# Performance work log

Hardware: AMD Instinct MI355X
Metric: run time of the kernel (lower is better)

## Reference

```python
import jax, jax.numpy as jnp
import numpy as np
from itertools import combinations

SEQ_LEN = 8
FEAT = 2048
SET_SIZE = 2
DOUT = 1152
WAY = 5
SHOT = 5
NQ = 500
MAX_LEN = int(SEQ_LEN * 1.5)
LN_EPS = 1e-5

TUPLES = np.array(list(combinations(range(SEQ_LEN), SET_SIZE)), dtype=np.int32)  # [T, SET_SIZE]
T_LEN = TUPLES.shape[0]  # C(8,2) = 28

def _positional_encoding(d_model, max_len):
    pos = np.arange(max_len, dtype=np.float32)[:, None]
    div = np.exp(np.arange(0, d_model, 2, dtype=np.float32) * (-np.log(10000.0) / d_model))
    pe = np.zeros((max_len, d_model), dtype=np.float32)
    pe[:, 0::2] = np.sin(pos * div)
    pe[:, 1::2] = np.cos(pos * div)
    return jnp.asarray(pe)

PE = _positional_encoding(FEAT, MAX_LEN)  # dropout is identity in eval mode

def _layernorm(x, gamma, beta):
    mu = jnp.mean(x, axis=-1, keepdims=True)
    var = jnp.var(x, axis=-1, keepdims=True)
    return (x - mu) * jax.lax.rsqrt(var + LN_EPS) * gamma + beta

def setup_inputs() -> dict:
    key = jax.random.key(0)
    ks = jax.random.split(key, 8)
    din = FEAT * SET_SIZE
    sc = 1.0 / np.sqrt(din)
    return {
        "support_set": jax.random.normal(ks[0], (WAY * SHOT, SEQ_LEN, FEAT), jnp.float32),
        "support_labels": jnp.repeat(jnp.arange(WAY, dtype=jnp.int32), SHOT),  # sorted, balanced episode
        "queries": jax.random.normal(ks[1], (NQ, SEQ_LEN, FEAT), jnp.float32),
        "k_w": jax.random.normal(ks[2], (din, DOUT), jnp.float32) * sc,
        "k_b": jnp.zeros((DOUT,), jnp.float32),
        "v_w": jax.random.normal(ks[3], (din, DOUT), jnp.float32) * sc,
        "v_b": jnp.zeros((DOUT,), jnp.float32),
        "ln_k_gamma": jnp.ones((DOUT,), jnp.float32),
        "ln_k_beta": jnp.zeros((DOUT,), jnp.float32),
        "global_temperature": jnp.asarray(1.0, jnp.float32),
        "temperature_weight": jnp.ones((1,), jnp.float32),
    }

def reference(support_set, support_labels, queries, k_w, k_b, v_w, v_b,
              ln_k_gamma, ln_k_beta, global_temperature, temperature_weight):
    n_q = queries.shape[0]
    # positional encoding (dropout is eval-mode identity)
    s = support_set + PE[:SEQ_LEN]
    q = queries + PE[:SEQ_LEN]
    # gather frame tuples: [n, T, SET_SIZE, FEAT] -> [n, T, SET_SIZE*FEAT]
    s_t = s[:, TUPLES, :].reshape(WAY * SHOT, T_LEN, SET_SIZE * FEAT)
    q_t = q[:, TUPLES, :].reshape(n_q, T_LEN, SET_SIZE * FEAT)
    # K / V projections; LayerNorm only on K (as in the module)
    s_ks = _layernorm(s_t @ k_w + k_b, ln_k_gamma, ln_k_beta)
    q_ks = _layernorm(q_t @ k_w + k_b, ln_k_gamma, ln_k_beta)
    s_vs = s_t @ v_w + v_b
    q_vs = q_t @ v_w + v_b
    # labels are sorted & balanced -> per-class slices are a reshape
    class_k = s_ks.reshape(WAY, SHOT, T_LEN, DOUT)
    class_v = s_vs.reshape(WAY, SHOT, T_LEN, DOUT)
    # scores[c,q,t,k,u] = <q_ks[q,t], class_k[c,k,u]> / sqrt(DOUT)
    scores = jnp.einsum('qtd,ckud->cqtku', q_ks, class_k) / np.sqrt(DOUT)
    # softmax jointly over (support-clip k, support-tuple u) per query tuple t
    attn = jax.nn.softmax(scores.reshape(WAY, n_q, T_LEN, SHOT * T_LEN), axis=-1)
    attn = attn.reshape(WAY, n_q, T_LEN, SHOT, T_LEN)
    # prototype = sum over support clips of attn @ class_v
    proto = jnp.einsum('cqtku,ckud->cqtd', attn, class_v)  # [WAY, NQ, T, DOUT]
    diff = q_vs[None] - proto
    dist = jnp.sum(diff * diff, axis=(-2, -1)) / T_LEN  # [WAY, NQ]
    logits = (-dist * global_temperature * temperature_weight[0]).T  # [NQ, WAY]
    return logits
```

## Files before the change

kernel.cpp:

```cpp
#include <hip/hip_runtime.h>

typedef __bf16 bf16;
typedef __attribute__((ext_vector_type(8))) __bf16 bf16x8;
typedef __attribute__((ext_vector_type(4))) float f32x4;

#define AS1 __attribute__((address_space(1)))
#define AS3 __attribute__((address_space(3)))

__device__ __constant__ int c_T0[28] = {0,0,0,0,0,0,0,1,1,1,1,1,1,2,2,2,2,2,3,3,3,3,4,4,4,5,5,6};
__device__ __constant__ int c_T1[28] = {1,2,3,4,5,6,7,2,3,4,5,6,7,3,4,5,6,7,4,5,6,7,5,6,7,6,7,7};

__global__ __launch_bounds__(256) void fill_pack(
    const float* __restrict__ queries, const float* __restrict__ support,
    const float* __restrict__ kw, const float* __restrict__ vw,
    bf16* __restrict__ X, bf16* __restrict__ Wp)
{
    __shared__ float t[32][33];
    const int tid = threadIdx.x;
    if (blockIdx.x < 4224) {
        const int f = blockIdx.x;
        bf16* row = X + (long)f * 2048;
        const int d0 = tid << 3;
        if (f >= 4200) {
            bf16x8 z;
            #pragma unroll
            for (int i = 0; i < 8; ++i) z[i] = (bf16)0.f;
            *(bf16x8*)(row + d0) = z;
            return;
        }
        const float* src = (f < 4000) ? (queries + (long)f * 2048)
                                      : (support + (long)(f - 4000) * 2048);
        const int s = f & 7;
        bf16x8 o;
        #pragma unroll
        for (int i = 0; i < 8; ++i) {
            int d = d0 + i;
            float dv = __expf((float)(d >> 1) * -0.008994473019508f);
            float ang = (float)s * dv;
            float pe = (d & 1) ? __cosf(ang) : __sinf(ang);
            o[i] = (bf16)(src[d] + pe);
        }
        *(bf16x8*)(row + d0) = o;
    } else {
        const int b = blockIdx.x - 4224;
        const int k0 = (b & 63) << 5, n0g = (b >> 6) << 5;
        const int tx = tid & 31, ty = tid >> 5;
        const int j = n0g / 1152, nc = n0g % 1152;
        const float* src = ((j < 2) ? kw : vw) + (long)(((j & 1) << 11) + k0) * 1152 + nc;
        #pragma unroll
        for (int i = 0; i < 4; ++i)
            t[ty + (i << 3)][tx] = src[(long)(ty + (i << 3)) * 1152 + tx];
        __syncthreads();
        #pragma unroll
        for (int i = 0; i < 4; ++i)
            Wp[(long)(n0g + ty + (i << 3)) * 2048 + k0 + tx] = (bf16)t[tx][ty + (i << 3)];
    }
}

template <typename OutT>
__global__ __launch_bounds__(256) void gemm_bt(
    const bf16* __restrict__ A, const bf16* __restrict__ A2,
    const bf16* __restrict__ A3, int split1, int split2,
    long lda, long lda3, const bf16* __restrict__ B, long ldb,
    OutT* __restrict__ C, int N, int K, float scale, int tiles_n)
{
    __shared__ __align__(16) bf16 lA[128 * 32];
    __shared__ __align__(16) bf16 lB[128 * 32];
    const int tid = threadIdx.x;
    const int wid = tid >> 6, lane = tid & 63;
    const int wm = (wid >> 1) << 6, wn = (wid & 1) << 6;
    const int quad = lane >> 4, l16 = lane & 15;
    const int nbm = gridDim.x / tiles_n;
    const int grp = 8 * tiles_n;
    const int gid = blockIdx.x / grp;
    const int first = gid << 3;
    const int gsz = min(8, nbm - first);
    const int pig = blockIdx.x % grp;
    const int tm = first + (pig % gsz);
    const int tn = pig / gsz;
    const int m0 = tm << 7, n0 = tn << 7;
    long la = lda;
    const bf16* Abase;
    if (tm < split1)       Abase = A  + (long)m0 * lda;
    else if (tm < split2)  Abase = A2 + (long)(m0 - (split1 << 7)) * lda;
    else                 { Abase = A3 + (long)(m0 - (split2 << 7)) * lda3; la = lda3; }

    f32x4 acc[4][4];
    #pragma unroll
    for (int i = 0; i < 4; ++i)
        #pragma unroll
        for (int j = 0; j < 4; ++j)
            #pragma unroll
            for (int r = 0; r < 4; ++r) acc[i][j][r] = 0.f;

    const int srow = lane >> 2, scol = (lane & 3) << 3;
    for (int kk = 0; kk < K; kk += 32) {
        __syncthreads();
        #pragma unroll
        for (int p = 0; p < 2; ++p) {
            const int rbase = (wid << 5) + (p << 4);
            const bf16* ga = Abase + (long)(rbase + srow) * la + kk + scol;
            const bf16* gb = B + (long)(n0 + rbase + srow) * ldb + kk + scol;
            __builtin_amdgcn_global_load_lds((const AS1 unsigned int*)ga,
                                             (AS3 unsigned int*)(lA + rbase * 32), 16, 0, 0);
            __builtin_amdgcn_global_load_lds((const AS1 unsigned int*)gb,
                                             (AS3 unsigned int*)(lB + rbase * 32), 16, 0, 0);
        }
        __builtin_amdgcn_s_waitcnt(0);
        __syncthreads();
        bf16x8 af[4], bfr[4];
        #pragma unroll
        for (int i = 0; i < 4; ++i)
            af[i] = *(const bf16x8*)(lA + (wm + (i << 4) + l16) * 32 + (quad << 3));
        #pragma unroll
        for (int j = 0; j < 4; ++j)
            bfr[j] = *(const bf16x8*)(lB + (wn + (j << 4) + l16) * 32 + (quad << 3));
        #pragma unroll
        for (int i = 0; i < 4; ++i)
            #pragma unroll
            for (int j = 0; j < 4; ++j)
                acc[i][j] = __builtin_amdgcn_mfma_f32_16x16x32_bf16(af[i], bfr[j], acc[i][j], 0, 0, 0);
    }
    #pragma unroll
    for (int i = 0; i < 4; ++i) {
        const int row = m0 + wm + (i << 4) + (quad << 2);
        #pragma unroll
        for (int j = 0; j < 4; ++j) {
            const int col = n0 + wn + (j << 4) + l16;
            OutT* cp = C + (long)row * N + col;
            #pragma unroll
            for (int r = 0; r < 4; ++r) cp[(long)r * N] = (OutT)(acc[i][j][r] * scale);
        }
    }
}

__global__ __launch_bounds__(256) void proj_rows(
    const bf16* __restrict__ H, const float* __restrict__ kb,
    const float* __restrict__ vb, const float* __restrict__ gamma,
    const float* __restrict__ beta,
    bf16* __restrict__ qks, bf16* __restrict__ sks, bf16* __restrict__ svs)
{
    const int bid = blockIdx.x, tid = threadIdx.x;
    bf16 *outK, *outV = nullptr;
    int fi = 0, fj = 0;
    bool valid;
    if (bid < 14080) {
        outK = qks + (long)bid * 1152;
        valid = (bid < 14000);
        if (valid) {
            int q = bid / 28, t = bid - q * 28;
            fi = (q << 3) + c_T0[t];
            fj = (q << 3) + c_T1[t];
        }
    } else {
        int m2 = bid - 14080;
        outK = sks + (long)m2 * 1152;
        outV = svs + (long)m2 * 1152;
        valid = (m2 < 700);
        if (valid) {
            int n = m2 / 28, t = m2 - n * 28;
            fi = 4000 + (n << 3) + c_T0[t];
            fj = 4000 + (n << 3) + c_T1[t];
        }
    }
    if (!valid) {
        for (int d = tid; d < 1152; d += 256) {
            outK[d] = (bf16)0.f;
            if (outV) outV[d] = (bf16)0.f;
        }
        return;
    }
    const bf16* Hi = H + (long)fi * 4608;
    const bf16* Hj = H + (long)fj * 4608;
    float xv[5];
    float sum = 0.f, sumsq = 0.f;
    #pragma unroll
    for (int it = 0; it < 5; ++it) {
        int d = tid + (it << 8);
        float x = 0.f;
        if (d < 1152) {
            x = (float)Hi[d] + (float)Hj[1152 + d] + kb[d];
            sum += x; sumsq += x * x;
        }
        xv[it] = x;
    }
    #pragma unroll
    for (int off = 32; off > 0; off >>= 1) {
        sum += __shfl_xor(sum, off, 64);
        sumsq += __shfl_xor(sumsq, off, 64);
    }
    __shared__ float s1[4], s2[4];
    const int wid = tid >> 6;
    if ((tid & 63) == 0) { s1[wid] = sum; s2[wid] = sumsq; }
    __syncthreads();
    sum = s1[0] + s1[1] + s1[2] + s1[3];
    sumsq = s2[0] + s2[1] + s2[2] + s2[3];
    const float mu = sum * (1.f / 1152.f);
    const float var = sumsq * (1.f / 1152.f) - mu * mu;
    const float rs = rsqrtf(var + 1e-5f);
    #pragma unroll
    for (int it = 0; it < 5; ++it) {
        int d = tid + (it << 8);
        if (d < 1152) outK[d] = (bf16)((xv[it] - mu) * rs * gamma[d] + beta[d]);
    }
    if (outV) {
        #pragma unroll
        for (int it = 0; it < 5; ++it) {
            int d = tid + (it << 8);
            if (d < 1152) outV[d] = (bf16)((float)Hi[2304 + d] + (float)Hj[3456 + d] + vb[d]);
        }
    }
}

__global__ __launch_bounds__(256) void qs_pair(
    const bf16* __restrict__ H, const float* __restrict__ vb, float* __restrict__ QS)
{
    const int q = blockIdx.x, tid = threadIdx.x;
    __shared__ __align__(16) bf16 Vt[8 * 1152];
    __shared__ __align__(16) bf16 Vb[8 * 1152];
    __shared__ float dots[64];
    for (int idx = tid; idx < 1152; idx += 256) {
        int row = idx / 144, col = (idx - row * 144) << 3;
        const bf16* src = H + (long)((q << 3) + row) * 4608;
        *(bf16x8*)(Vt + row * 1152 + col) = *(const bf16x8*)(src + 2304 + col);
        *(bf16x8*)(Vb + row * 1152 + col) = *(const bf16x8*)(src + 3456 + col);
    }
    __syncthreads();
    const int wid = tid >> 6, lane = tid & 63;
    for (int task = wid; task <= 60; task += 4) {
        float s = 0.f;
        if (task == 60) {
            for (int c = lane << 3; c < 1152; c += 512) {
                #pragma unroll
                for (int k = 0; k < 8; ++k) { float v = vb[c + k]; s += v * v; }
            }
        } else if (task < 16) {
            const bf16* p = (task < 8) ? (Vt + task * 1152) : (Vb + (task - 8) * 1152);
            for (int c = lane << 3; c < 1152; c += 512) {
                bf16x8 v = *(const bf16x8*)(p + c);
                #pragma unroll
                for (int k = 0; k < 8; ++k) { float f = (float)v[k]; s += f * f; }
            }
        } else if (task < 32) {
            const bf16* p = (task < 24) ? (Vt + (task - 16) * 1152) : (Vb + (task - 24) * 1152);
            for (int c = lane << 3; c < 1152; c += 512) {
                bf16x8 v = *(const bf16x8*)(p + c);
                #pragma unroll
                for (int k = 0; k < 8; ++k) s += (float)v[k] * vb[c + k];
            }
        } else {
            int t = task - 32;
            const bf16* pa = Vt + c_T0[t] * 1152;
            const bf16* pb = Vb + c_T1[t] * 1152;
            for (int c = lane << 3; c < 1152; c += 512) {
                bf16x8 a = *(const bf16x8*)(pa + c);
                bf16x8 b = *(const bf16x8*)(pb + c);
                #pragma unroll
                for (int k = 0; k < 8; ++k) s += (float)a[k] * (float)b[k];
            }
        }
        #pragma unroll
        for (int off = 32; off > 0; off >>= 1) s += __shfl_xor(s, off, 64);
        if (lane == 0) dots[task] = s;
    }
    __syncthreads();
    if (tid < 64) {
        float term = 0.f;
        if (lane < 28) {
            int i = c_T0[lane], j = c_T1[lane];
            term = dots[i] + dots[8 + j] + dots[60]
                 + 2.f * (dots[32 + lane] + dots[16 + i] + dots[24 + j]);
        }
        #pragma unroll
        for (int off = 32; off > 0; off >>= 1) term += __shfl_xor(term, off, 64);
        if (lane == 0) QS[q] = term;
    }
}

__global__ __launch_bounds__(256) void small_ops(
    const float* __restrict__ Gf, bf16* __restrict__ Gb,
    const float* __restrict__ vb, const bf16* __restrict__ svs,
    float* __restrict__ bdot)
{
    if (blockIdx.x < 2304) {
        int i = blockIdx.x * 256 + threadIdx.x;
        int r = i / 768, col = i - r * 768;
        bool keep = (r < 700) && (col < 700) && (r / 140 == col / 140);
        Gb[i] = keep ? (bf16)Gf[i] : (bf16)0.f;
    } else {
        const int u = ((blockIdx.x - 2304) << 2) + (threadIdx.x >> 6);
        const int lane = threadIdx.x & 63;
        const bf16* p = svs + (long)u * 1152;
        float s = 0.f;
        for (int d = lane; d < 1152; d += 64) s += vb[d] * (float)p[d];
        #pragma unroll
        for (int off = 32; off > 0; off >>= 1) s += __shfl_xor(s, off, 64);
        if (lane == 0) bdot[u] = s;
    }
}

__global__ __launch_bounds__(320) void softmax_attn(
    const float* __restrict__ scores, bf16* __restrict__ attn)
{
    const int m = blockIdx.x, tid = threadIdx.x;
    bf16* arow = attn + (long)m * 768;
    if (m >= 14000) {
        for (int d = tid; d < 768; d += 320) arow[d] = (bf16)0.f;
        return;
    }
    if (tid < 68) arow[700 + tid] = (bf16)0.f;
    const int w = tid >> 6, lane = tid & 63;
    const float* srow = scores + (long)m * 768 + w * 140;
    float v0 = srow[lane];
    float v1 = srow[64 + lane];
    float v2 = (lane < 12) ? srow[128 + lane] : -1e30f;
    float mx = fmaxf(fmaxf(v0, v1), v2);
    #pragma unroll
    for (int off = 32; off > 0; off >>= 1) mx = fmaxf(mx, __shfl_xor(mx, off, 64));
    float e0 = __expf(v0 - mx), e1 = __expf(v1 - mx);
    float e2 = (lane < 12) ? __expf(v2 - mx) : 0.f;
    float s = e0 + e1 + e2;
    #pragma unroll
    for (int off = 32; off > 0; off >>= 1) s += __shfl_xor(s, off, 64);
    const float inv = 1.f / s;
    bf16* aw = arow + w * 140;
    aw[lane] = (bf16)(e0 * inv);
    aw[64 + lane] = (bf16)(e1 * inv);
    if (lane < 12) aw[128 + lane] = (bf16)(e2 * inv);
}

__global__ __launch_bounds__(256) void final_dist(
    const bf16* __restrict__ attn, const bf16* __restrict__ attnG,
    const float* __restrict__ Fv, const float* __restrict__ bdot,
    float* __restrict__ dist)
{
    const int w = threadIdx.x >> 6, lane = threadIdx.x & 63;
    const int m = blockIdx.x * 4 + w;
    const int q = m / 28, t = m - q * 28;
    const int fi = (q << 3) + c_T0[t], fj = (q << 3) + c_T1[t];
    const bf16* ar = attn + (long)m * 768;
    const bf16* gr = attnG + (long)m * 768;
    const float* ft = Fv + (long)fi * 768;
    const float* fb = Fv + (long)(4224 + fj) * 768;
    #pragma unroll
    for (int c = 0; c < 5; ++c) {
        const int base = c * 140;
        float s = 0.f;
        {
            int u = base + lane;
            float wv = ft[u] + fb[u] + bdot[u];
            s += (float)ar[u] * ((float)gr[u] - 2.f * wv);
        }
        {
            int u = base + 64 + lane;
            float wv = ft[u] + fb[u] + bdot[u];
            s += (float)ar[u] * ((float)gr[u] - 2.f * wv);
        }
        if (lane < 12) {
            int u = base + 128 + lane;
            float wv = ft[u] + fb[u] + bdot[u];
            s += (float)ar[u] * ((float)gr[u] - 2.f * wv);
        }
        #pragma unroll
        for (int off = 32; off > 0; off >>= 1) s += __shfl_xor(s, off, 64);
        if (lane == 0) atomicAdd(&dist[c * 500 + q], s);
    }
}

__global__ void finalize(const float* __restrict__ dist, const float* __restrict__ QS,
                         const float* __restrict__ gt, const float* __restrict__ tw,
                         float* __restrict__ out)
{
    int i = blockIdx.x * 256 + threadIdx.x;
    if (i < 2500) {
        int q = i / 5, c = i - q * 5;
        out[i] = -(dist[c * 500 + q] + QS[q]) * (gt[0] * tw[0] * (1.f / 28.f));
    }
}

extern "C" void kernel_launch(void* const* d_in, const int* in_sizes, int n_in,
                              void* d_out, int out_size, void* d_ws, size_t ws_size,
                              hipStream_t stream)
{
    const float* support = (const float*)d_in[0];
    const float* queries = (const float*)d_in[2];
    const float* kw      = (const float*)d_in[3];
    const float* kb      = (const float*)d_in[4];
    const float* vw      = (const float*)d_in[5];
    const float* vb      = (const float*)d_in[6];
    const float* gamma   = (const float*)d_in[7];
    const float* beta    = (const float*)d_in[8];
    const float* gt      = (const float*)d_in[9];
    const float* tw      = (const float*)d_in[10];
    float* out = (float*)d_out;

    const int BIG = 1 << 20;

    char* ws = (char*)d_ws;
    size_t off = 0;
    auto alloc = [&](size_t b) { char* p = ws + off; off += (b + 255) & ~(size_t)255; return p; };
    bf16* X      = (bf16*)alloc(4224ull * 2048 * 2);
    bf16* Wp     = (bf16*)alloc(4608ull * 2048 * 2);
    char* uni    = alloc(14080ull * 768 * 4);
    bf16* H      = (bf16*)uni;
    float* scores= (float*)uni;
    bf16* qks    = (bf16*)alloc(14080ull * 1152 * 2);
    bf16* attnG  = (bf16*)qks;
    bf16* sks    = (bf16*)alloc(768ull * 1152 * 2);
    bf16* svs    = (bf16*)alloc(768ull * 1152 * 2);
    bf16* attn   = (bf16*)alloc(14080ull * 768 * 2);
    float* Fv    = (float*)alloc(9216ull * 768 * 4);
    float* Gf    = Fv + 8448ull * 768;
    bf16* Gb     = (bf16*)alloc(768ull * 768 * 2);
    float* bdot  = (float*)alloc(768 * 4);
    float* QS    = (float*)alloc(500 * 4);
    float* dist  = (float*)alloc(5 * 500 * 4);

    hipMemsetAsync(dist, 0, 5 * 500 * 4, stream);
    fill_pack<<<4224 + 9216, 256, 0, stream>>>(queries, support, kw, vw, X, Wp);
    gemm_bt<bf16><<<33 * 36, 256, 0, stream>>>(X, X, X, BIG, BIG, 2048, 2048, Wp, 2048,
                                               H, 4608, 2048, 1.f, 36);
    proj_rows<<<14848, 256, 0, stream>>>(H, kb, vb, gamma, beta, qks, sks, svs);
    qs_pair<<<500, 256, 0, stream>>>(H, vb, QS);
    gemm_bt<float><<<72 * 6, 256, 0, stream>>>(H + 2304, H + 3456, svs, 33, 66, 4608, 1152,
                                               svs, 1152, Fv, 768, 1152, 1.f, 6);
    small_ops<<<2304 + 192, 256, 0, stream>>>(Gf, Gb, vb, svs, bdot);
    gemm_bt<float><<<110 * 6, 256, 0, stream>>>(qks, qks, qks, BIG, BIG, 1152, 1152, sks, 1152,
                                                scores, 768, 1152, 0.029462782549439484f, 6);
    softmax_attn<<<14080, 320, 0, stream>>>(scores, attn);
    gemm_bt<bf16><<<110 * 6, 256, 0, stream>>>(attn, attn, attn, BIG, BIG, 768, 768, Gb, 768,
                                               attnG, 768, 768, 1.f, 6);
    final_dist<<<3500, 256, 0, stream>>>(attn, attnG, Fv, bdot, dist);
    finalize<<<10, 256, 0, stream>>>(dist, QS, gt, tw, out);
}
```

Measured before the change: 458.5 us.

## Compute query K scores per frame, then assemble LayerNorm-folded scores per tuple

Drops the per-tuple query K materialization and the 14000x768x1152 score GEMM. The LayerNorm on query K is expanded algebraically: scores come from per-frame GEMMs against gamma-scaled support keys, combined with per-row mean and rstd from a row_stats kernel and per-support bias dot products. The frame GEMMs and the support Gram GEMM are merged into one launch that writes the masked Gram directly. This removes a large GEMM and the qks write, at the cost of extra stats kernels and possible numerical drift from computing variance as E[x^2]-mu^2 from bf16 partial sums.

```diff
diff --git a/kernel.cpp b/kernel.cpp
--- a/kernel.cpp
+++ b/kernel.cpp
@@ -59,9 +59,7 @@
 
 template <typename OutT>
 __global__ __launch_bounds__(256) void gemm_bt(
-    const bf16* __restrict__ A, const bf16* __restrict__ A2,
-    const bf16* __restrict__ A3, int split1, int split2,
-    long lda, long lda3, const bf16* __restrict__ B, long ldb,
+    const bf16* __restrict__ A, long lda, const bf16* __restrict__ B, long ldb,
     OutT* __restrict__ C, int N, int K, float scale, int tiles_n)
 {
     __shared__ __align__(16) bf16 lA[128 * 32];
@@ -70,20 +68,9 @@
     const int wid = tid >> 6, lane = tid & 63;
     const int wm = (wid >> 1) << 6, wn = (wid & 1) << 6;
     const int quad = lane >> 4, l16 = lane & 15;
-    const int nbm = gridDim.x / tiles_n;
-    const int grp = 8 * tiles_n;
-    const int gid = blockIdx.x / grp;
-    const int first = gid << 3;
-    const int gsz = min(8, nbm - first);
-    const int pig = blockIdx.x % grp;
-    const int tm = first + (pig % gsz);
-    const int tn = pig / gsz;
+    const int tm = blockIdx.x / tiles_n, tn = blockIdx.x % tiles_n;
     const int m0 = tm << 7, n0 = tn << 7;
-    long la = lda;
-    const bf16* Abase;
-    if (tm < split1)       Abase = A  + (long)m0 * lda;
-    else if (tm < split2)  Abase = A2 + (long)(m0 - (split1 << 7)) * lda;
-    else                 { Abase = A3 + (long)(m0 - (split2 << 7)) * lda3; la = lda3; }
+    const bf16* Abase = A + (long)m0 * lda;
 
     f32x4 acc[4][4];
     #pragma unroll
@@ -99,7 +86,7 @@
         #pragma unroll
         for (int p = 0; p < 2; ++p) {
             const int rbase = (wid << 5) + (p << 4);
-            const bf16* ga = Abase + (long)(rbase + srow) * la + kk + scol;
+            const bf16* ga = Abase + (long)(rbase + srow) * lda + kk + scol;
             const bf16* gb = B + (long)(n0 + rbase + srow) * ldb + kk + scol;
             __builtin_amdgcn_global_load_lds((const AS1 unsigned int*)ga,
                                              (AS3 unsigned int*)(lA + rbase * 32), 16, 0, 0);
@@ -134,42 +121,112 @@
     }
 }
 
-__global__ __launch_bounds__(256) void proj_rows(
+__global__ __launch_bounds__(256) void gemm_frames(
+    const bf16* __restrict__ H, const bf16* __restrict__ Bk,
+    const bf16* __restrict__ svs, float* __restrict__ FG, bf16* __restrict__ Gb)
+{
+    __shared__ __align__(16) bf16 lA[128 * 32];
+    __shared__ __align__(16) bf16 lB[128 * 32];
+    const int tid = threadIdx.x;
+    const int wid = tid >> 6, lane = tid & 63;
+    const int wm = (wid >> 1) << 6, wn = (wid & 1) << 6;
+    const int quad = lane >> 4, l16 = lane & 15;
+    const bool gram = (int)blockIdx.x >= 792;
+    int seg = 4, tm, tn;
+    const bf16* Abase;
+    long la;
+    const bf16* B;
+    if (!gram) {
+        seg = blockIdx.x / 198;
+        int r = blockIdx.x % 198;
+        tm = r / 6; tn = r % 6;
+        Abase = H + seg * 1152 + (long)(tm << 7) * 4608;
+        la = 4608;
+        B = (seg < 2) ? Bk : svs;
+    } else {
+        int r = blockIdx.x - 792;
+        tm = r / 6; tn = r % 6;
+        Abase = svs + (long)(tm << 7) * 1152;
+        la = 1152;
+        B = svs;
+    }
+    const int n0 = tn << 7;
+
+    f32x4 acc[4][4];
+    #pragma unroll
+    for (int i = 0; i < 4; ++i)
+        #pragma unroll
+        for (int j = 0; j < 4; ++j)
+            #pragma unroll
+            for (int r = 0; r < 4; ++r) acc[i][j][r] = 0.f;
+
+    const int srow = lane >> 2, scol = (lane & 3) << 3;
+    for (int kk = 0; kk < 1152; kk += 32) {
+        __syncthreads();
+        #pragma unroll
+        for (int p = 0; p < 2; ++p) {
+            const int rbase = (wid << 5) + (p << 4);
+            const bf16* ga = Abase + (long)(rbase + srow) * la + kk + scol;
+            const bf16* gb = B + (long)(n0 + rbase + srow) * 1152 + kk + scol;
+            __builtin_amdgcn_global_load_lds((const AS1 unsigned int*)ga,
+                                             (AS3 unsigned int*)(lA + rbase * 32), 16, 0, 0);
+            __builtin_amdgcn_global_load_lds((const AS1 unsigned int*)gb,
+                                             (AS3 unsigned int*)(lB + rbase * 32), 16, 0, 0);
+        }
+        __builtin_amdgcn_s_waitcnt(0);
+        __syncthreads();
+        bf16x8 af[4], bfr[4];
+        #pragma unroll
+        for (int i = 0; i < 4; ++i)
+            af[i] = *(const bf16x8*)(lA + (wm + (i << 4) + l16) * 32 + (quad << 3));
+        #pragma unroll
+        for (int j = 0; j < 4; ++j)
+            bfr[j] = *(const bf16x8*)(lB + (wn + (j << 4) + l16) * 32 + (quad << 3));
+        #pragma unroll
+        for (int i = 0; i < 4; ++i)
+            #pragma unroll
+            for (int j = 0; j < 4; ++j)
+                acc[i][j] = __builtin_amdgcn_mfma_f32_16x16x32_bf16(af[i], bfr[j], acc[i][j], 0, 0, 0);
+    }
+    #pragma unroll
+    for (int i = 0; i < 4; ++i) {
+        const int rloc = (tm << 7) + wm + (i << 4) + (quad << 2);
+        #pragma unroll
+        for (int j = 0; j < 4; ++j) {
+            const int col = n0 + wn + (j << 4) + l16;
+            #pragma unroll
+            for (int r = 0; r < 4; ++r) {
+                const int row = rloc + r;
+                if (!gram) {
+                    FG[(long)(seg * 4224 + row) * 768 + col] = acc[i][j][r];
+                } else {
+                    bool keep = (row < 700) && (col < 700) && (row / 140 == col / 140);
+                    Gb[(long)row * 768 + col] = keep ? (bf16)acc[i][j][r] : (bf16)0.f;
+                }
+            }
+        }
+    }
+}
+
+__global__ __launch_bounds__(256) void proj_support(
     const bf16* __restrict__ H, const float* __restrict__ kb,
     const float* __restrict__ vb, const float* __restrict__ gamma,
     const float* __restrict__ beta,
-    bf16* __restrict__ qks, bf16* __restrict__ sks, bf16* __restrict__ svs)
-{
-    const int bid = blockIdx.x, tid = threadIdx.x;
-    bf16 *outK, *outV = nullptr;
-    int fi = 0, fj = 0;
-    bool valid;
-    if (bid < 14080) {
-        outK = qks + (long)bid * 1152;
-        valid = (bid < 14000);
-        if (valid) {
-            int q = bid / 28, t = bid - q * 28;
-            fi = (q << 3) + c_T0[t];
-            fj = (q << 3) + c_T1[t];
-        }
-    } else {
-        int m2 = bid - 14080;
-        outK = sks + (long)m2 * 1152;
-        outV = svs + (long)m2 * 1152;
-        valid = (m2 < 700);
-        if (valid) {
-            int n = m2 / 28, t = m2 - n * 28;
-            fi = 4000 + (n << 3) + c_T0[t];
-            fj = 4000 + (n << 3) + c_T1[t];
-        }
-    }
-    if (!valid) {
-        for (int d = tid; d < 1152; d += 256) {
-            outK[d] = (bf16)0.f;
-            if (outV) outV[d] = (bf16)0.f;
-        }
+    bf16* __restrict__ Bk, bf16* __restrict__ svs,
+    float* __restrict__ gd, float* __restrict__ kbd,
+    float* __restrict__ bd2, float* __restrict__ bdot)
+{
+    const int u = blockIdx.x, tid = threadIdx.x;
+    bf16* outK = Bk + (long)u * 1152;
+    bf16* outV = svs + (long)u * 1152;
+    if (u >= 700) {
+        for (int d = tid; d < 1152; d += 256) { outK[d] = (bf16)0.f; outV[d] = (bf16)0.f; }
+        if (tid == 0) { gd[u] = 0.f; kbd[u] = 0.f; bd2[u] = 0.f; bdot[u] = 0.f; }
         return;
     }
+    const int n = u / 28, t = u - n * 28;
+    const int fi = 4000 + (n << 3) + c_T0[t];
+    const int fj = 4000 + (n << 3) + c_T1[t];
     const bf16* Hi = H + (long)fi * 4608;
     const bf16* Hj = H + (long)fj * 4608;
     float xv[5];
@@ -189,7 +246,7 @@
         sum += __shfl_xor(sum, off, 64);
         sumsq += __shfl_xor(sumsq, off, 64);
     }
-    __shared__ float s1[4], s2[4];
+    __shared__ float s1[4], s2[4], sr[4][4];
     const int wid = tid >> 6;
     if ((tid & 63) == 0) { s1[wid] = sum; s2[wid] = sumsq; }
     __syncthreads();
@@ -198,109 +255,131 @@
     const float mu = sum * (1.f / 1152.f);
     const float var = sumsq * (1.f / 1152.f) - mu * mu;
     const float rs = rsqrtf(var + 1e-5f);
+    float g_ = 0.f, k_ = 0.f, b_ = 0.f, v_ = 0.f;
     #pragma unroll
     for (int it = 0; it < 5; ++it) {
         int d = tid + (it << 8);
-        if (d < 1152) outK[d] = (bf16)((xv[it] - mu) * rs * gamma[d] + beta[d]);
-    }
-    if (outV) {
-        #pragma unroll
-        for (int it = 0; it < 5; ++it) {
-            int d = tid + (it << 8);
-            if (d < 1152) outV[d] = (bf16)((float)Hi[2304 + d] + (float)Hj[3456 + d] + vb[d]);
-        }
-    }
-}
-
-__global__ __launch_bounds__(256) void qs_pair(
-    const bf16* __restrict__ H, const float* __restrict__ vb, float* __restrict__ QS)
-{
-    const int q = blockIdx.x, tid = threadIdx.x;
-    __shared__ __align__(16) bf16 Vt[8 * 1152];
-    __shared__ __align__(16) bf16 Vb[8 * 1152];
-    __shared__ float dots[64];
+        if (d < 1152) {
+            float gm = gamma[d];
+            float sk = (xv[it] - mu) * rs * gm + beta[d];
+            outK[d] = (bf16)(gm * sk);
+            g_ += gm * sk;
+            k_ += kb[d] * gm * sk;
+            b_ += beta[d] * sk;
+            float sv = (float)Hi[2304 + d] + (float)Hj[3456 + d] + vb[d];
+            outV[d] = (bf16)sv;
+            v_ += vb[d] * sv;
+        }
+    }
+    #pragma unroll
+    for (int off = 32; off > 0; off >>= 1) {
+        g_ += __shfl_xor(g_, off, 64);
+        k_ += __shfl_xor(k_, off, 64);
+        b_ += __shfl_xor(b_, off, 64);
+        v_ += __shfl_xor(v_, off, 64);
+    }
+    if ((tid & 63) == 0) { sr[wid][0] = g_; sr[wid][1] = k_; sr[wid][2] = b_; sr[wid][3] = v_; }
+    __syncthreads();
+    if (tid == 0) {
+        gd[u]   = sr[0][0] + sr[1][0] + sr[2][0] + sr[3][0];
+        kbd[u]  = sr[0][1] + sr[1][1] + sr[2][1] + sr[3][1];
+        bd2[u]  = sr[0][2] + sr[1][2] + sr[2][2] + sr[3][2];
+        bdot[u] = sr[0][3] + sr[1][3] + sr[2][3] + sr[3][3];
+    }
+}
+
+__global__ __launch_bounds__(256) void row_stats(
+    const bf16* __restrict__ H, const float* __restrict__ kb,
+    const float* __restrict__ vb, float* __restrict__ MU,
+    float* __restrict__ RS, float* __restrict__ QS)
+{
+    const bool kside = (int)blockIdx.x < 500;
+    const int q = kside ? blockIdx.x : blockIdx.x - 500;
+    const int co = kside ? 0 : 2304;
+    const float* bias = kside ? kb : vb;
+    const int tid = threadIdx.x;
+    __shared__ __align__(16) bf16 Ft[8 * 1152];
+    __shared__ __align__(16) bf16 Fb[8 * 1152];
+    __shared__ float Sa[8], Qa[8], Ca[8], Sb_[8], Qb_[8], Cb_[8], Pp[28], Sk2[2];
     for (int idx = tid; idx < 1152; idx += 256) {
         int row = idx / 144, col = (idx - row * 144) << 3;
-        const bf16* src = H + (long)((q << 3) + row) * 4608;
-        *(bf16x8*)(Vt + row * 1152 + col) = *(const bf16x8*)(src + 2304 + col);
-        *(bf16x8*)(Vb + row * 1152 + col) = *(const bf16x8*)(src + 3456 + col);
+        const bf16* src = H + (long)((q << 3) + row) * 4608 + co;
+        *(bf16x8*)(Ft + row * 1152 + col) = *(const bf16x8*)(src + col);
+        *(bf16x8*)(Fb + row * 1152 + col) = *(const bf16x8*)(src + 1152 + col);
     }
     __syncthreads();
     const int wid = tid >> 6, lane = tid & 63;
-    for (int task = wid; task <= 60; task += 4) {
-        float s = 0.f;
-        if (task == 60) {
-            for (int c = lane << 3; c < 1152; c += 512) {
-                #pragma unroll
-                for (int k = 0; k < 8; ++k) { float v = vb[c + k]; s += v * v; }
-            }
-        } else if (task < 16) {
-            const bf16* p = (task < 8) ? (Vt + task * 1152) : (Vb + (task - 8) * 1152);
+    for (int task = wid; task < 45; task += 4) {
+        float s0 = 0.f, s1 = 0.f, s2 = 0.f;
+        if (task < 16) {
+            const bf16* p = (task < 8) ? (Ft + task * 1152) : (Fb + (task - 8) * 1152);
             for (int c = lane << 3; c < 1152; c += 512) {
                 bf16x8 v = *(const bf16x8*)(p + c);
                 #pragma unroll
-                for (int k = 0; k < 8; ++k) { float f = (float)v[k]; s += f * f; }
+                for (int k = 0; k < 8; ++k) {
+                    float f = (float)v[k];
+                    s0 += f; s1 += f * f; s2 += f * bias[c + k];
+                }
             }
-        } else if (task < 32) {
-            const bf16* p = (task < 24) ? (Vt + (task - 16) * 1152) : (Vb + (task - 24) * 1152);
-            for (int c = lane << 3; c < 1152; c += 512) {
-                bf16x8 v = *(const bf16x8*)(p + c);
-                #pragma unroll
-                for (int k = 0; k < 8; ++k) s += (float)v[k] * vb[c + k];
-            }
-        } else {
-            int t = task - 32;
-            const bf16* pa = Vt + c_T0[t] * 1152;
-            const bf16* pb = Vb + c_T1[t] * 1152;
+        } else if (task < 44) {
+            int t = task - 16;
+            const bf16* pa = Ft + c_T0[t] * 1152;
+            const bf16* pb = Fb + c_T1[t] * 1152;
             for (int c = lane << 3; c < 1152; c += 512) {
                 bf16x8 a = *(const bf16x8*)(pa + c);
                 bf16x8 b = *(const bf16x8*)(pb + c);
                 #pragma unroll
-                for (int k = 0; k < 8; ++k) s += (float)a[k] * (float)b[k];
+                for (int k = 0; k < 8; ++k) s0 += (float)a[k] * (float)b[k];
             }
-        }
-        #pragma unroll
-        for (int off = 32; off > 0; off >>= 1) s += __shfl_xor(s, off, 64);
-        if (lane == 0) dots[task] = s;
+        } else {
+            for (int c = lane << 3; c < 1152; c += 512) {
+                #pragma unroll
+                for (int k = 0; k < 8; ++k) { float f = bias[c + k]; s0 += f; s1 += f * f; }
+            }
+        }
+        #pragma unroll
+        for (int off = 32; off > 0; off >>= 1) {
+            s0 += __shfl_xor(s0, off, 64);
+            s1 += __shfl_xor(s1, off, 64);
+            s2 += __shfl_xor(s2, off, 64);
+        }
+        if (lane == 0) {
+            if (task < 8)       { Sa[task] = s0; Qa[task] = s1; Ca[task] = s2; }
+            else if (task < 16) { Sb_[task - 8] = s0; Qb_[task - 8] = s1; Cb_[task - 8] = s2; }
+            else if (task < 44) Pp[task - 16] = s0;
+            else                { Sk2[0] = s0; Sk2[1] = s1; }
+        }
     }
     __syncthreads();
-    if (tid < 64) {
-        float term = 0.f;
-        if (lane < 28) {
-            int i = c_T0[lane], j = c_T1[lane];
-            term = dots[i] + dots[8 + j] + dots[60]
-                 + 2.f * (dots[32 + lane] + dots[16 + i] + dots[24 + j]);
-        }
-        #pragma unroll
-        for (int off = 32; off > 0; off >>= 1) term += __shfl_xor(term, off, 64);
-        if (lane == 0) QS[q] = term;
-    }
-}
-
-__global__ __launch_bounds__(256) void small_ops(
-    const float* __restrict__ Gf, bf16* __restrict__ Gb,
-    const float* __restrict__ vb, const bf16* __restrict__ svs,
-    float* __restrict__ bdot)
-{
-    if (blockIdx.x < 2304) {
-        int i = blockIdx.x * 256 + threadIdx.x;
-        int r = i / 768, col = i - r * 768;
-        bool keep = (r < 700) && (col < 700) && (r / 140 == col / 140);
-        Gb[i] = keep ? (bf16)Gf[i] : (bf16)0.f;
+    if (kside) {
+        if (tid < 28) {
+            int i = c_T0[tid], j = c_T1[tid];
+            float mu = (Sa[i] + Sb_[j] + Sk2[0]) * (1.f / 1152.f);
+            float ex2 = (Qa[i] + Qb_[j] + Sk2[1] + 2.f * (Pp[tid] + Ca[i] + Cb_[j])) * (1.f / 1152.f);
+            float var = ex2 - mu * mu;
+            int m = q * 28 + tid;
+            MU[m] = mu;
+            RS[m] = rsqrtf(var + 1e-5f);
+        }
     } else {
-        const int u = ((blockIdx.x - 2304) << 2) + (threadIdx.x >> 6);
-        const int lane = threadIdx.x & 63;
-        const bf16* p = svs + (long)u * 1152;
-        float s = 0.f;
-        for (int d = lane; d < 1152; d += 64) s += vb[d] * (float)p[d];
-        #pragma unroll
-        for (int off = 32; off > 0; off >>= 1) s += __shfl_xor(s, off, 64);
-        if (lane == 0) bdot[u] = s;
-    }
-}
-
-__global__ __launch_bounds__(320) void softmax_attn(
-    const float* __restrict__ scores, bf16* __restrict__ attn)
+        if (tid < 64) {
+            float term = 0.f;
+            if (lane < 28) {
+                int i = c_T0[lane], j = c_T1[lane];
+                term = Qa[i] + Qb_[j] + Sk2[1] + 2.f * (Pp[lane] + Ca[i] + Cb_[j]);
+            }
+            #pragma unroll
+            for (int off = 32; off > 0; off >>= 1) term += __shfl_xor(term, off, 64);
+            if (lane == 0) QS[q] = term;
+        }
+    }
+}
+
+__global__ __launch_bounds__(320) void assemble_softmax(
+    const float* __restrict__ Fkt, const float* __restrict__ Fkb,
+    const float* __restrict__ MU, const float* __restrict__ RS,
+    const float* __restrict__ gd, const float* __restrict__ kbd,
+    const float* __restrict__ bd2, bf16* __restrict__ attn)
 {
     const int m = blockIdx.x, tid = threadIdx.x;
     bf16* arow = attn + (long)m * 768;
@@ -309,11 +388,19 @@
         return;
     }
     if (tid < 68) arow[700 + tid] = (bf16)0.f;
+    const int q = m / 28, t = m - q * 28;
+    const float* ft = Fkt + (long)((q << 3) + c_T0[t]) * 768;
+    const float* fb = Fkb + (long)((q << 3) + c_T1[t]) * 768;
+    const float mu = MU[m], rs = RS[m];
     const int w = tid >> 6, lane = tid & 63;
-    const float* srow = scores + (long)m * 768 + w * 140;
-    float v0 = srow[lane];
-    float v1 = srow[64 + lane];
-    float v2 = (lane < 12) ? srow[128 + lane] : -1e30f;
+    const int base = w * 140;
+    const float sc = 0.029462782549439484f;
+    int u0 = base + lane, u1 = base + 64 + lane, u2 = base + 128 + lane;
+    float v0 = (rs * (ft[u0] + fb[u0] + kbd[u0] - mu * gd[u0]) + bd2[u0]) * sc;
+    float v1 = (rs * (ft[u1] + fb[u1] + kbd[u1] - mu * gd[u1]) + bd2[u1]) * sc;
+    float v2 = (lane < 12)
+             ? (rs * (ft[u2] + fb[u2] + kbd[u2] - mu * gd[u2]) + bd2[u2]) * sc
+             : -1e30f;
     float mx = fmaxf(fmaxf(v0, v1), v2);
     #pragma unroll
     for (int off = 32; off > 0; off >>= 1) mx = fmaxf(mx, __shfl_xor(mx, off, 64));
@@ -323,7 +410,7 @@
     #pragma unroll
     for (int off = 32; off > 0; off >>= 1) s += __shfl_xor(s, off, 64);
     const float inv = 1.f / s;
-    bf16* aw = arow + w * 140;
+    bf16* aw = arow + base;
     aw[lane] = (bf16)(e0 * inv);
     aw[64 + lane] = (bf16)(e1 * inv);
     if (lane < 12) aw[128 + lane] = (bf16)(e2 * inv);
@@ -331,7 +418,7 @@
 
 __global__ __launch_bounds__(256) void final_dist(
     const bf16* __restrict__ attn, const bf16* __restrict__ attnG,
-    const float* __restrict__ Fv, const float* __restrict__ bdot,
+    const float* __restrict__ FG, const float* __restrict__ bdot,
     float* __restrict__ dist)
 {
     const int w = threadIdx.x >> 6, lane = threadIdx.x & 63;
@@ -340,8 +427,8 @@
     const int fi = (q << 3) + c_T0[t], fj = (q << 3) + c_T1[t];
     const bf16* ar = attn + (long)m * 768;
     const bf16* gr = attnG + (long)m * 768;
-    const float* ft = Fv + (long)fi * 768;
-    const float* fb = Fv + (long)(4224 + fj) * 768;
+    const float* ft = FG + (long)(8448 + fi) * 768;
+    const float* fb = FG + (long)(12672 + fj) * 768;
     #pragma unroll
     for (int c = 0; c < 5; ++c) {
         const int base = c * 140;
@@ -394,8 +481,6 @@
     const float* tw      = (const float*)d_in[10];
     float* out = (float*)d_out;
 
-    const int BIG = 1 << 20;
-
     char* ws = (char*)d_ws;
     size_t off = 0;
     auto alloc = [&](size_t b) { char* p = ws + off; off += (b + 255) & ~(size_t)255; return p; };
@@ -403,33 +488,29 @@
     bf16* Wp     = (bf16*)alloc(4608ull * 2048 * 2);
     char* uni    = alloc(14080ull * 768 * 4);
     bf16* H      = (bf16*)uni;
-    float* scores= (float*)uni;
-    bf16* qks    = (bf16*)alloc(14080ull * 1152 * 2);
-    bf16* attnG  = (bf16*)qks;
-    bf16* sks    = (bf16*)alloc(768ull * 1152 * 2);
+    bf16* attn   = (bf16*)uni;
+    bf16* attnG  = (bf16*)(uni + 14080ull * 768 * 2);
+    float* FG    = (float*)alloc(16896ull * 768 * 4);
+    bf16* Bk     = (bf16*)alloc(768ull * 1152 * 2);
     bf16* svs    = (bf16*)alloc(768ull * 1152 * 2);
-    bf16* attn   = (bf16*)alloc(14080ull * 768 * 2);
-    float* Fv    = (float*)alloc(9216ull * 768 * 4);
-    float* Gf    = Fv + 8448ull * 768;
     bf16* Gb     = (bf16*)alloc(768ull * 768 * 2);
+    float* MU    = (float*)alloc(14000ull * 4);
+    float* RS    = (float*)alloc(14000ull * 4);
+    float* gd    = (float*)alloc(768 * 4);
+    float* kbd   = (float*)alloc(768 * 4);
+    float* bd2   = (float*)alloc(768 * 4);
     float* bdot  = (float*)alloc(768 * 4);
     float* QS    = (float*)alloc(500 * 4);
     float* dist  = (float*)alloc(5 * 500 * 4);
 
     hipMemsetAsync(dist, 0, 5 * 500 * 4, stream);
     fill_pack<<<4224 + 9216, 256, 0, stream>>>(queries, support, kw, vw, X, Wp);
-    gemm_bt<bf16><<<33 * 36, 256, 0, stream>>>(X, X, X, BIG, BIG, 2048, 2048, Wp, 2048,
-                                               H, 4608, 2048, 1.f, 36);
-    proj_rows<<<14848, 256, 0, stream>>>(H, kb, vb, gamma, beta, qks, sks, svs);
-    qs_pair<<<500, 256, 0, stream>>>(H, vb, QS);
-    gemm_bt<float><<<72 * 6, 256, 0, stream>>>(H + 2304, H + 3456, svs, 33, 66, 4608, 1152,
-                                               svs, 1152, Fv, 768, 1152, 1.f, 6);
-    small_ops<<<2304 + 192, 256, 0, stream>>>(Gf, Gb, vb, svs, bdot);
-    gemm_bt<float><<<110 * 6, 256, 0, stream>>>(qks, qks, qks, BIG, BIG, 1152, 1152, sks, 1152,
-                                                scores, 768, 1152, 0.029462782549439484f, 6);
-    softmax_attn<<<14080, 320, 0, stream>>>(scores, attn);
-    gemm_bt<bf16><<<110 * 6, 256, 0, stream>>>(attn, attn, attn, BIG, BIG, 768, 768, Gb, 768,
-                                               attnG, 768, 768, 1.f, 6);
-    final_dist<<<3500, 256, 0, stream>>>(attn, attnG, Fv, bdot, dist);
+    gemm_bt<bf16><<<33 * 36, 256, 0, stream>>>(X, 2048, Wp, 2048, H, 4608, 2048, 1.f, 36);
+    proj_support<<<768, 256, 0, stream>>>(H, kb, vb, gamma, beta, Bk, svs, gd, kbd, bd2, bdot);
+    row_stats<<<1000, 256, 0, stream>>>(H, kb, vb, MU, RS, QS);
+    gemm_frames<<<828, 256, 0, stream>>>(H, Bk, svs, FG, Gb);
+    assemble_softmax<<<14080, 320, 0, stream>>>(FG, FG + 4224ull * 768, MU, RS, gd, kbd, bd2, attn);
+    gemm_bt<bf16><<<110 * 6, 256, 0, stream>>>(attn, 768, Gb, 768, attnG, 768, 768, 1.f, 6);
+    final_dist<<<3500, 256, 0, stream>>>(attn, attnG, FG, bdot, dist);
     finalize<<<10, 256, 0, stream>>>(dist, QS, gt, tw, out);
 }
```

Result: faster. 423.5 us (-7.6%).
